# Performance work log

Hardware: AMD Instinct MI355X
Metric: run time of the kernel (lower is better)

## Reference

```python
import jax, jax.numpy as jnp
import numpy as np

N = 4096
D = 2048   # latent_dim
H = 2048   # projector hidden
P = 128    # projection dim
TEMP = 0.1
SIGMA = 5.0
GAMMA = 1.0 / (2.0 * SIGMA ** 2)
INF = 1.0e8
BN_EPS = 1e-5


def setup_inputs() -> dict:
    key = jax.random.key(0)
    k1, k2, k3, k4, k5 = jax.random.split(key, 5)
    return {
        "y1": jax.random.normal(k1, (N, D), jnp.float32),
        "y2": jax.random.normal(k2, (N, D), jnp.float32),
        "labels": jax.random.normal(k3, (N,), jnp.float32),
        "W1": jax.random.normal(k4, (H, D), jnp.float32) * 0.02,
        "bn_gamma": jnp.ones((H,), jnp.float32),
        "bn_beta": jnp.zeros((H,), jnp.float32),
        "W2": jax.random.normal(k5, (P, H), jnp.float32) * 0.02,
    }


def _project(x, W1, bn_gamma, bn_beta, W2):
    # Linear(no bias) -> BatchNorm1d (training: batch stats, biased var) -> ReLU -> Linear(no bias)
    h = x @ W1.T                                   # [N, H]
    mu = jnp.mean(h, axis=0)
    var = jnp.mean((h - mu) ** 2, axis=0)          # biased variance, as torch BN
    h = (h - mu) * jax.lax.rsqrt(var + BN_EPS) * bn_gamma + bn_beta
    h = jax.nn.relu(h)
    return h @ W2.T                                # [N, P]


def reference(y1, y2, labels, W1, bn_gamma, bn_beta, W2):
    z_i = _project(y1, W1, bn_gamma, bn_beta, W2)
    z_j = _project(y2, W1, bn_gamma, bn_beta, W2)
    n = z_i.shape[0]

    # L2 normalize
    z_i = z_i / jnp.linalg.norm(z_i, axis=-1, keepdims=True)
    z_j = z_j / jnp.linalg.norm(z_j, axis=-1, keepdims=True)

    eye_n = jnp.eye(n, dtype=z_i.dtype)
    sim_zii = z_i @ z_i.T / TEMP - INF * eye_n     # [N, N]
    sim_zjj = z_j @ z_j.T / TEMP - INF * eye_n
    sim_zij = z_i @ z_j.T / TEMP

    # RBF kernel weights over duplicated labels (sigma > 0 path)
    all_labels = jnp.concatenate([labels, labels]).reshape(2 * n, -1)   # [2N, L]
    sq_dist = jnp.sum((all_labels[:, None, :] - all_labels[None, :, :]) ** 2, axis=-1)
    weights = jnp.exp(-GAMMA * sq_dist)            # [2N, 2N]
    weights = weights * (1.0 - jnp.eye(2 * n, dtype=weights.dtype))
    weights = weights / jnp.sum(weights, axis=1, keepdims=True)

    sim_Z = jnp.concatenate([
        jnp.concatenate([sim_zii, sim_zij], axis=1),
        jnp.concatenate([sim_zij.T, sim_zjj], axis=1),
    ], axis=0)                                     # [2N, 2N]
    log_sim_Z = jax.nn.log_softmax(sim_Z, axis=1)
    loss = -jnp.sum(weights * log_sim_Z) / n
    return loss
```

## Files before the change

kernel.cpp:

```cpp
#include <hip/hip_runtime.h>

typedef unsigned short u16;
typedef unsigned int   u32;
typedef float  f32x4  __attribute__((ext_vector_type(4)));
typedef short  s16x8  __attribute__((ext_vector_type(8)));
typedef __bf16 bf16x8 __attribute__((ext_vector_type(8)));

#define GAMMA_C 0.02f
#define NSPLIT 16

__device__ __forceinline__ float bf2f(u16 h) {
  union { u32 u; float f; } c; c.u = ((u32)h) << 16; return c.f;
}
__device__ __forceinline__ u16 f2bf(float f) {
  union { float f; u32 u; } c; c.f = f;
  u32 u = c.u;
  return (u16)((u + 0x7fffu + ((u >> 16) & 1u)) >> 16);
}
__device__ __forceinline__ f32x4 mfma16(s16x8 a, s16x8 b, f32x4 c) {
  union { s16x8 s; bf16x8 b; } ua, ub; ua.s = a; ub.s = b;
  return __builtin_amdgcn_mfma_f32_16x16x32_bf16(ua.b, ub.b, c, 0, 0, 0);
}
__device__ __forceinline__ void gload_lds16(const void* g, void* l) {
  __builtin_amdgcn_global_load_lds(
      (__attribute__((address_space(1))) const void*)g,
      (__attribute__((address_space(3))) void*)l, 16, 0, 0);
}

__global__ __launch_bounds__(256)
void castall(const float* __restrict__ y1, const float* __restrict__ y2,
             const float* __restrict__ W1, const float* __restrict__ W2,
             u16* __restrict__ Ybf, u16* __restrict__ W1bf,
             u16* __restrict__ W2bf, float* __restrict__ zbuf) {
  int b = blockIdx.x;
  if (b >= 10368) {
    int i = ((b - 10368) * 256 + threadIdx.x) * 4;
    *(float4*)(zbuf + i) = make_float4(0.f, 0.f, 0.f, 0.f);
    return;
  }
  const float* src; u16* dst; int off;
  if (b < 4096)       { src = y1; dst = Ybf;           off = b; }
  else if (b < 8192)  { src = y2; dst = Ybf + 8388608; off = b - 4096; }
  else if (b < 10240) { src = W1; dst = W1bf;          off = b - 8192; }
  else                { src = W2; dst = W2bf;          off = b - 10240; }
  int idx = (off * 256 + threadIdx.x) * 8;
  float4 a = *(const float4*)(src + idx);
  float4 c = *(const float4*)(src + idx + 4);
  int4 ov; u16* op = (u16*)&ov;
  op[0]=f2bf(a.x); op[1]=f2bf(a.y); op[2]=f2bf(a.z); op[3]=f2bf(a.w);
  op[4]=f2bf(c.x); op[5]=f2bf(c.y); op[6]=f2bf(c.z); op[7]=f2bf(c.w);
  *(int4*)(dst + idx) = ov;
}

#define SWZ1(row) (((row) & 7) << 4)
#define BAR() __builtin_amdgcn_s_barrier()
#define VMW0() asm volatile("s_waitcnt vmcnt(0)" ::: "memory")

#define STAGE_T(BUF, KT) do {                                                      \
  _Pragma("unroll")                                                                \
  for (int c_ = 0; c_ < 4; ++c_) {                                                 \
    int e_ = tid + c_*512; int row_ = e_ >> 3; int b_ = (e_ & 7) * 16;             \
    int bs_ = b_ ^ SWZ1(row_);                                                     \
    gload_lds16((const char*)A + (size_t)(tm+row_)*4096 + (KT)*2 + bs_,            \
                (char*)&As[BUF][0] + (c_*512 + wave*64)*16);                       \
    gload_lds16((const char*)B + (size_t)(tn+row_)*4096 + (KT)*2 + bs_,            \
                (char*)&Bs[BUF][0] + (c_*512 + wave*64)*16);                       \
  }                                                                                \
} while (0)

#define LDA(DST, BUF, MH) do {                                                     \
  _Pragma("unroll")                                                                \
  for (int m_ = 0; m_ < 4; ++m_)                                                   \
    _Pragma("unroll")                                                              \
    for (int kk_ = 0; kk_ < 2; ++kk_) {                                            \
      int arow_ = wr*16 + ((MH)*4 + m_)*32 + r16;                                  \
      DST[m_*2 + kk_] = *(const s16x8*)((const char*)&As[BUF][0] + arow_*128 +     \
                          ((kk_*64 + g*16) ^ SWZ1(arow_)));                        \
    }                                                                              \
} while (0)

#define LDB(DST, BUF, NH) do {                                                     \
  _Pragma("unroll")                                                                \
  for (int n_ = 0; n_ < 2; ++n_)                                                   \
    _Pragma("unroll")                                                              \
    for (int kk_ = 0; kk_ < 2; ++kk_) {                                            \
      int brow_ = wc*16 + ((NH)*2 + n_)*64 + r16;                                  \
      DST[n_*2 + kk_] = *(const s16x8*)((const char*)&Bs[BUF][0] + brow_*128 +     \
                          ((kk_*64 + g*16) ^ SWZ1(brow_)));                        \
    }                                                                              \
} while (0)

#define MMQ(AF, MH, NH) do {                                                       \
  __builtin_amdgcn_s_setprio(1);                                                   \
  _Pragma("unroll")                                                                \
  for (int m_ = 0; m_ < 4; ++m_)                                                   \
    _Pragma("unroll")                                                              \
    for (int n_ = 0; n_ < 2; ++n_)                                                 \
      _Pragma("unroll")                                                            \
      for (int kk_ = 0; kk_ < 2; ++kk_)                                            \
        acc[(MH)*4 + m_][(NH)*2 + n_] =                                            \
          mfma16(AF[m_*2 + kk_], bv[n_*2 + kk_], acc[(MH)*4 + m_][(NH)*2 + n_]);   \
  __builtin_amdgcn_s_setprio(0);                                                   \
} while (0)

__global__ __launch_bounds__(512, 2)
void gemm1(const u16* __restrict__ A, const u16* __restrict__ B,
           u16* __restrict__ C, float* __restrict__ psum, float* __restrict__ psumsq)
{
  __shared__ u16 As[2][256*64];
  __shared__ u16 Bs[2][256*64];
  const int tid = threadIdx.x;
  const int lane = tid & 63, wave = tid >> 6;
  const int wr = wave >> 2, wc = wave & 3;
  const int g = lane >> 4, r16 = lane & 15;
  const int lin = blockIdx.x;
  const int wgid = (lin & 7) * 32 + (lin >> 3);
  const int by = wgid >> 3, bx = wgid & 7;
  const int tm = by * 256, tn = bx * 256;

  f32x4 acc[8][4] = {};
  s16x8 af0[8], af1[8], bv[4];

  STAGE_T(0, 0);
  VMW0(); BAR();

  for (int t = 0; t < 32; ++t) {
    const int cur = t & 1, nxt = cur ^ 1;
    const int ktn = (t + 1) * 64;
    LDA(af0, cur, 0);  LDB(bv, cur, 0);
    if (t < 31) STAGE_T(nxt, ktn);
    BAR();  MMQ(af0, 0, 0);  BAR();
    LDA(af1, cur, 1);
    BAR();  MMQ(af1, 1, 0);  BAR();
    LDB(bv, cur, 1);
    BAR();  MMQ(af1, 1, 1);  BAR();
    if (t < 31) VMW0();
    BAR();  MMQ(af0, 0, 1);  BAR();
  }

  #pragma unroll
  for (int m = 0; m < 8; ++m)
    #pragma unroll
    for (int n = 0; n < 4; ++n)
      #pragma unroll
      for (int r = 0; r < 4; ++r) {
        int row = tm + wr*16 + m*32 + g*4 + r;
        int col = tn + wc*16 + n*64 + r16;
        C[(size_t)row*2048 + col] = f2bf(acc[m][n][r]);
      }

  __syncthreads();
  float* sred  = (float*)&As[0][0];
  float* ssred = sred + 512;
  #pragma unroll
  for (int n = 0; n < 4; ++n) {
    float s = 0.f, ss = 0.f;
    #pragma unroll
    for (int m = 0; m < 8; ++m)
      #pragma unroll
      for (int r = 0; r < 4; ++r) { float v = acc[m][n][r]; s += v; ss = fmaf(v, v, ss); }
    s  += __shfl_xor(s, 16);  s  += __shfl_xor(s, 32);
    ss += __shfl_xor(ss, 16); ss += __shfl_xor(ss, 32);
    if (g == 0) {
      int lc = wc*16 + n*64 + r16;
      sred [wr*256 + lc] = s;
      ssred[wr*256 + lc] = ss;
    }
  }
  __syncthreads();
  if (tid < 256) {
    int half = tm >> 12;
    atomicAdd(&psum  [half*2048 + tn + tid], sred [tid] + sred [256 + tid]);
    atomicAdd(&psumsq[half*2048 + tn + tid], ssred[tid] + ssred[256 + tid]);
  }
}

__global__ __launch_bounds__(256)
void bnfinal(const float* __restrict__ psum, const float* __restrict__ psumsq,
             const float* __restrict__ gam, const float* __restrict__ bet,
             float* __restrict__ scale, float* __restrict__ bias)
{
  int c = blockIdx.x * 256 + threadIdx.x;
  int col = c & 2047;
  float mu  = psum[c] * (1.f/4096.f);
  float var = fmaxf(psumsq[c] * (1.f/4096.f) - mu*mu, 0.f);
  float sc = gam[col] * rsqrtf(var + 1e-5f);
  scale[c] = sc;
  bias [c] = bet[col] - mu * sc;
}

__global__ __launch_bounds__(256)
void gemm2f(const u16* __restrict__ Hraw, const u16* __restrict__ W2bf,
            const float* __restrict__ scale, const float* __restrict__ bias,
            u16* __restrict__ Zp, int kLen)
{
  __shared__ u16 As[128*64];
  __shared__ u16 Bs[128*64];
  const int tid = threadIdx.x;
  const int lane = tid & 63, wave = tid >> 6;
  const int wr = wave >> 1, wc = wave & 1;
  const int g = lane >> 4, r16 = lane & 15;
  const int tm = blockIdx.y * 128, tn = blockIdx.x * 128;
  const int kOff = blockIdx.z * kLen;
  const float* scp = scale + (size_t)(tm >> 12) * 2048;
  const float* bip = bias  + (size_t)(tm >> 12) * 2048;

  f32x4 acc[4][4] = {};

  for (int kt = kOff; kt < kOff + kLen; kt += 64) {
    #pragma unroll
    for (int c = 0; c < 4; ++c) {
      int ld = (tid + c*256) * 16;
      int row = ld >> 7, b = ld & 127;
      int bs = b ^ ((row & 7) << 4);
      gload_lds16((const char*)W2bf + (size_t)(tn+row)*4096 + (kt*2 + bs),
                  (char*)Bs + (wave*64 + c*256)*16);
    }
    #pragma unroll
    for (int c = 0; c < 4; ++c) {
      int ld = (tid + c*256) * 16;
      int row = ld >> 7, b = ld & 127;
      int kg = kt + (b >> 1);
      int4 hv = *(const int4*)((const char*)Hraw + (size_t)(tm+row)*4096 + kt*2 + b);
      f32x4 s0 = *(const f32x4*)(scp + kg), s1 = *(const f32x4*)(scp + kg + 4);
      f32x4 b0 = *(const f32x4*)(bip + kg), b1 = *(const f32x4*)(bip + kg + 4);
      u16* hp = (u16*)&hv;
      int4 ov; u16* op = (u16*)&ov;
      #pragma unroll
      for (int j = 0; j < 4; ++j)
        op[j]   = f2bf(fmaxf(fmaf(bf2f(hp[j]),   s0[j], b0[j]), 0.f));
      #pragma unroll
      for (int j = 0; j < 4; ++j)
        op[4+j] = f2bf(fmaxf(fmaf(bf2f(hp[4+j]), s1[j], b1[j]), 0.f));
      *(int4*)((char*)As + row*128 + (b ^ ((row & 7) << 4))) = ov;
    }
    __syncthreads();
    #pragma unroll
    for (int kk = 0; kk < 2; ++kk) {
      s16x8 af[4], bv[4];
      #pragma unroll
      for (int m = 0; m < 4; ++m) {
        int row = wr*64 + m*16 + r16;
        af[m] = *(const s16x8*)((const char*)As + row*128 +
                                ((kk*64 + g*16) ^ ((row & 7) << 4)));
      }
      #pragma unroll
      for (int n = 0; n < 4; ++n) {
        int row = wc*64 + n*16 + r16;
        bv[n] = *(const s16x8*)((const char*)Bs + row*128 +
                                ((kk*64 + g*16) ^ ((row & 7) << 4)));
      }
      #pragma unroll
      for (int m = 0; m < 4; ++m)
        #pragma unroll
        for (int n = 0; n < 4; ++n)
          acc[m][n] = mfma16(af[m], bv[n], acc[m][n]);
    }
    __syncthreads();
  }

  u16* Cfo = Zp + (size_t)blockIdx.z * (8192*128);
  #pragma unroll
  for (int m = 0; m < 4; ++m)
    #pragma unroll
    for (int n = 0; n < 4; ++n)
      #pragma unroll
      for (int r = 0; r < 4; ++r) {
        int row = tm + wr*64 + m*16 + g*4 + r;
        int col = tn + wc*64 + n*16 + r16;
        Cfo[(size_t)row*128 + col] = f2bf(acc[m][n][r]);
      }
}

__global__ __launch_bounds__(256)
void normk(const u16* __restrict__ Zp, u16* __restrict__ Zb)
{
  int row = blockIdx.x * 16 + (threadIdx.x >> 4);
  int l16 = threadIdx.x & 15;
  size_t off = (size_t)row*128 + l16*8;
  f32x4 v0 = {0.f,0.f,0.f,0.f}, v1 = {0.f,0.f,0.f,0.f};
  #pragma unroll
  for (int s = 0; s < 8; ++s) {
    int4 pv = *(const int4*)(Zp + (size_t)s*1048576 + off);
    const u16* pp = (const u16*)&pv;
    v0[0] += bf2f(pp[0]); v0[1] += bf2f(pp[1]); v0[2] += bf2f(pp[2]); v0[3] += bf2f(pp[3]);
    v1[0] += bf2f(pp[4]); v1[1] += bf2f(pp[5]); v1[2] += bf2f(pp[6]); v1[3] += bf2f(pp[7]);
  }
  float ss = v0[0]*v0[0] + v0[1]*v0[1] + v0[2]*v0[2] + v0[3]*v0[3]
           + v1[0]*v1[0] + v1[1]*v1[1] + v1[2]*v1[2] + v1[3]*v1[3];
  #pragma unroll
  for (int o = 1; o < 16; o <<= 1) ss += __shfl_xor(ss, o);
  float rs = rsqrtf(ss);
  rs = rs * (1.5f - 0.5f * ss * rs * rs);
  int4 ov; u16* op = (u16*)&ov;
  op[0]=f2bf(v0[0]*rs); op[1]=f2bf(v0[1]*rs); op[2]=f2bf(v0[2]*rs); op[3]=f2bf(v0[3]*rs);
  op[4]=f2bf(v1[0]*rs); op[5]=f2bf(v1[1]*rs); op[6]=f2bf(v1[2]*rs); op[7]=f2bf(v1[3]*rs);
  *(int4*)((char*)Zb + off*2) = ov;
}

#define LOAD_COL(DC, DL, IT) do {                                                  \
  int jr_ = colBase + (IT)*16;                                                     \
  const char* zcp_ = (const char*)Zb + (size_t)(jr_ + r16)*256 + g*16;             \
  DC[0] = *(const s16x8*)(zcp_);        DC[1] = *(const s16x8*)(zcp_ +  64);       \
  DC[2] = *(const s16x8*)(zcp_ + 128);  DC[3] = *(const s16x8*)(zcp_ + 192);       \
  DL = *(const f32x4*)(labels + ((jr_ & 4095) + g*4));                             \
} while (0)

#define LBODY(CC, CL, IT) do {                                                     \
  int jrow_ = colBase + (IT)*16;                                                   \
  f32x4 acc0 = {0.f,0.f,0.f,0.f};                                                  \
  f32x4 acc1 = {0.f,0.f,0.f,0.f};                                                  \
  acc0 = mfma16(CC[0], zr[0][0], acc0);                                            \
  acc0 = mfma16(CC[1], zr[0][1], acc0);                                            \
  acc0 = mfma16(CC[2], zr[0][2], acc0);                                            \
  acc0 = mfma16(CC[3], zr[0][3], acc0);                                            \
  acc1 = mfma16(CC[0], zr[1][0], acc1);                                            \
  acc1 = mfma16(CC[1], zr[1][1], acc1);                                            \
  acc1 = mfma16(CC[2], zr[1][2], acc1);                                            \
  acc1 = mfma16(CC[3], zr[1][3], acc1);                                            \
  _Pragma("unroll")                                                                \
  for (int r = 0; r < 4; ++r) {                                                    \
    int j = jrow_ + g*4 + r;                                                       \
    _Pragma("unroll")                                                              \
    for (int is = 0; is < 2; ++is) {                                               \
      float d = (is ? acc1[r] : acc0[r]);                                          \
      bool diag = (rowBase + is*16 + r16) == j;                                    \
      float e  = __expf(fmaf(d, 10.f, -10.f));                                     \
      float dl = li[is] - CL[r];                                                   \
      float w  = __expf(-GAMMA_C * dl * dl);                                       \
      e = diag ? 0.f : e;                                                          \
      w = diag ? 0.f : w;                                                          \
      l[is] += e;                                                                  \
      wS[is] += w;                                                                 \
      wA[is] = fmaf(w, d, wA[is]);                                                 \
    }                                                                              \
  }                                                                                \
} while (0)

__global__ __launch_bounds__(64)
void lossk(const u16* __restrict__ Zb, const float* __restrict__ labels,
           float* __restrict__ lacc, float* __restrict__ wacc,
           float* __restrict__ sacc)
{
  const int lane = threadIdx.x & 63;
  const int g = lane >> 4, r16 = lane & 15;
  const int split = blockIdx.x;
  const int rowBase = blockIdx.y * 32;
  const int colBase = split * 512;

  s16x8 zr[2][4];
  float li[2];
  #pragma unroll
  for (int is = 0; is < 2; ++is) {
    int i = rowBase + is*16 + r16;
    li[is] = labels[i & 4095];
    #pragma unroll
    for (int kk = 0; kk < 4; ++kk)
      zr[is][kk] = *(const s16x8*)((const char*)Zb + (size_t)i*256 + kk*64 + g*16);
  }

  float l[2]  = {0.f, 0.f};
  float wA[2] = {0.f, 0.f};
  float wS[2] = {0.f, 0.f};

  s16x8 cA[4], cB[4];
  f32x4 lA, lB;
  LOAD_COL(cA, lA, 0);
  for (int it = 0; it < 32; it += 2) {
    LOAD_COL(cB, lB, it + 1);
    LBODY(cA, lA, it);
    if (it + 2 < 32) LOAD_COL(cA, lA, it + 2);
    LBODY(cB, lB, it + 1);
  }

  #pragma unroll
  for (int is = 0; is < 2; ++is) {
    float lv = l[is], wv = wA[is], sv = wS[is];
    lv += __shfl_xor(lv, 16); lv += __shfl_xor(lv, 32);
    wv += __shfl_xor(wv, 16); wv += __shfl_xor(wv, 32);
    sv += __shfl_xor(sv, 16); sv += __shfl_xor(sv, 32);
    if (g == 0) {
      int i = rowBase + is*16 + r16;
      atomicAdd(&lacc[i], lv);
      atomicAdd(&wacc[i], wv);
      atomicAdd(&sacc[i], sv);
    }
  }
}

__global__ __launch_bounds__(256)
void finalk(const float* __restrict__ lacc, const float* __restrict__ wacc,
            const float* __restrict__ sacc, float* __restrict__ out)
{
  __shared__ float red[256];
  float a = 0.f;
  for (int i = threadIdx.x; i < 8192; i += 256)
    a += wacc[i] * 10.f / sacc[i] - (10.f + logf(lacc[i]));
  red[threadIdx.x] = a;
  __syncthreads();
  for (int off = 128; off > 0; off >>= 1) {
    if (threadIdx.x < off) red[threadIdx.x] += red[threadIdx.x + off];
    __syncthreads();
  }
  if (threadIdx.x == 0) out[0] = -red[0] * (1.f/4096.f);
}

extern "C" void kernel_launch(void* const* d_in, const int* in_sizes, int n_in,
                              void* d_out, int out_size, void* d_ws, size_t ws_size,
                              hipStream_t stream) {
  const float* y1     = (const float*)d_in[0];
  const float* y2     = (const float*)d_in[1];
  const float* labels = (const float*)d_in[2];
  const float* W1     = (const float*)d_in[3];
  const float* bng    = (const float*)d_in[4];
  const float* bnb    = (const float*)d_in[5];
  const float* W2     = (const float*)d_in[6];
  float* out = (float*)d_out;
  char* ws = (char*)d_ws;

  u16*   Ybf    = (u16*)(ws);
  u16*   W1bf   = (u16*)(ws + 33554432);
  float* zbuf   = (float*)(ws + 41943040);
  float* psum   = (float*)(ws + 41943040);
  float* psumsq = (float*)(ws + 41959424);
  float* lacc   = (float*)(ws + 41975808);
  float* wacc   = (float*)(ws + 42008576);
  float* sacc   = (float*)(ws + 42041344);
  u16*   W2bf   = (u16*)(ws + 42074112);
  u16*   Hraw   = (u16*)(ws + 42598400);
  u16*   Zp     = (u16*)(ws + 32768);
  float* scale  = (float*)(ws + 33554432);
  float* biasv  = (float*)(ws + 33570816);
  u16*   Zbf    = (u16*)(ws + 33587200);

  castall<<<10400, 256, 0, stream>>>(y1, y2, W1, W2, Ybf, W1bf, W2bf, zbuf);
  gemm1<<<256, 512, 0, stream>>>(Ybf, W1bf, Hraw, psum, psumsq);
  bnfinal<<<16, 256, 0, stream>>>(psum, psumsq, bng, bnb, scale, biasv);
  gemm2f<<<dim3(1,64,8), 256, 0, stream>>>(Hraw, W2bf, scale, biasv, Zp, 256);
  normk<<<512, 256, 0, stream>>>(Zp, Zbf);
  lossk<<<dim3(NSPLIT, 256), 64, 0, stream>>>(Zbf, labels, lacc, wacc, sacc);
  finalk<<<1, 256, 0, stream>>>(lacc, wacc, sacc, out);
}
```

Measured before the change: 187.2 us.

## Fuse BN finalize into gemm2 prologue and widen loss kernel row tile

Removes the separate bnfinal launch: each gemm2f block now computes BN scale/bias for its 256-wide K slice from psum/psumsq into shared memory and reads them from LDS instead of global. Separately, the loss kernel now processes 64 rows per block (4 row subtiles) instead of 32, so each loaded column fragment feeds twice as many MFMAs and the grid halves. The cost is redundant BN computation across blocks, more registers per lane in lossk, and half as many loss blocks to spread over the CUs.

```diff
diff --git a/kernel.cpp b/kernel.cpp
--- a/kernel.cpp
+++ b/kernel.cpp
@@ -176,34 +176,31 @@
 }
 
 __global__ __launch_bounds__(256)
-void bnfinal(const float* __restrict__ psum, const float* __restrict__ psumsq,
-             const float* __restrict__ gam, const float* __restrict__ bet,
-             float* __restrict__ scale, float* __restrict__ bias)
-{
-  int c = blockIdx.x * 256 + threadIdx.x;
-  int col = c & 2047;
-  float mu  = psum[c] * (1.f/4096.f);
-  float var = fmaxf(psumsq[c] * (1.f/4096.f) - mu*mu, 0.f);
-  float sc = gam[col] * rsqrtf(var + 1e-5f);
-  scale[c] = sc;
-  bias [c] = bet[col] - mu * sc;
-}
-
-__global__ __launch_bounds__(256)
 void gemm2f(const u16* __restrict__ Hraw, const u16* __restrict__ W2bf,
-            const float* __restrict__ scale, const float* __restrict__ bias,
+            const float* __restrict__ psum, const float* __restrict__ psumsq,
+            const float* __restrict__ gam, const float* __restrict__ bet,
             u16* __restrict__ Zp, int kLen)
 {
   __shared__ u16 As[128*64];
   __shared__ u16 Bs[128*64];
+  __shared__ float sLDS[256], bLDS[256];
   const int tid = threadIdx.x;
   const int lane = tid & 63, wave = tid >> 6;
   const int wr = wave >> 1, wc = wave & 1;
   const int g = lane >> 4, r16 = lane & 15;
   const int tm = blockIdx.y * 128, tn = blockIdx.x * 128;
   const int kOff = blockIdx.z * kLen;
-  const float* scp = scale + (size_t)(tm >> 12) * 2048;
-  const float* bip = bias  + (size_t)(tm >> 12) * 2048;
+  const int half = tm >> 12;
+
+  {
+    int c = half*2048 + kOff + tid;
+    float mu  = psum[c] * (1.f/4096.f);
+    float var = fmaxf(psumsq[c] * (1.f/4096.f) - mu*mu, 0.f);
+    float sc = gam[kOff + tid] * rsqrtf(var + 1e-5f);
+    sLDS[tid] = sc;
+    bLDS[tid] = bet[kOff + tid] - mu * sc;
+  }
+  __syncthreads();
 
   f32x4 acc[4][4] = {};
 
@@ -220,10 +217,10 @@
     for (int c = 0; c < 4; ++c) {
       int ld = (tid + c*256) * 16;
       int row = ld >> 7, b = ld & 127;
-      int kg = kt + (b >> 1);
+      int kg = (kt - kOff) + (b >> 1);
       int4 hv = *(const int4*)((const char*)Hraw + (size_t)(tm+row)*4096 + kt*2 + b);
-      f32x4 s0 = *(const f32x4*)(scp + kg), s1 = *(const f32x4*)(scp + kg + 4);
-      f32x4 b0 = *(const f32x4*)(bip + kg), b1 = *(const f32x4*)(bip + kg + 4);
+      f32x4 s0 = *(const f32x4*)(sLDS + kg), s1 = *(const f32x4*)(sLDS + kg + 4);
+      f32x4 b0 = *(const f32x4*)(bLDS + kg), b1 = *(const f32x4*)(bLDS + kg + 4);
       u16* hp = (u16*)&hv;
       int4 ov; u16* op = (u16*)&ov;
       #pragma unroll
@@ -308,22 +305,19 @@
 
 #define LBODY(CC, CL, IT) do {                                                     \
   int jrow_ = colBase + (IT)*16;                                                   \
-  f32x4 acc0 = {0.f,0.f,0.f,0.f};                                                  \
-  f32x4 acc1 = {0.f,0.f,0.f,0.f};                                                  \
-  acc0 = mfma16(CC[0], zr[0][0], acc0);                                            \
-  acc0 = mfma16(CC[1], zr[0][1], acc0);                                            \
-  acc0 = mfma16(CC[2], zr[0][2], acc0);                                            \
-  acc0 = mfma16(CC[3], zr[0][3], acc0);                                            \
-  acc1 = mfma16(CC[0], zr[1][0], acc1);                                            \
-  acc1 = mfma16(CC[1], zr[1][1], acc1);                                            \
-  acc1 = mfma16(CC[2], zr[1][2], acc1);                                            \
-  acc1 = mfma16(CC[3], zr[1][3], acc1);                                            \
+  f32x4 aacc[4] = {};                                                              \
+  _Pragma("unroll")                                                                \
+  for (int kk = 0; kk < 4; ++kk) {                                                 \
+    _Pragma("unroll")                                                              \
+    for (int is = 0; is < 4; ++is)                                                 \
+      aacc[is] = mfma16(CC[kk], zr[is][kk], aacc[is]);                             \
+  }                                                                                \
   _Pragma("unroll")                                                                \
   for (int r = 0; r < 4; ++r) {                                                    \
     int j = jrow_ + g*4 + r;                                                       \
     _Pragma("unroll")                                                              \
-    for (int is = 0; is < 2; ++is) {                                               \
-      float d = (is ? acc1[r] : acc0[r]);                                          \
+    for (int is = 0; is < 4; ++is) {                                               \
+      float d = aacc[is][r];                                                       \
       bool diag = (rowBase + is*16 + r16) == j;                                    \
       float e  = __expf(fmaf(d, 10.f, -10.f));                                     \
       float dl = li[is] - CL[r];                                                   \
@@ -345,13 +339,13 @@
   const int lane = threadIdx.x & 63;
   const int g = lane >> 4, r16 = lane & 15;
   const int split = blockIdx.x;
-  const int rowBase = blockIdx.y * 32;
+  const int rowBase = blockIdx.y * 64;
   const int colBase = split * 512;
 
-  s16x8 zr[2][4];
-  float li[2];
-  #pragma unroll
-  for (int is = 0; is < 2; ++is) {
+  s16x8 zr[4][4];
+  float li[4];
+  #pragma unroll
+  for (int is = 0; is < 4; ++is) {
     int i = rowBase + is*16 + r16;
     li[is] = labels[i & 4095];
     #pragma unroll
@@ -359,9 +353,9 @@
       zr[is][kk] = *(const s16x8*)((const char*)Zb + (size_t)i*256 + kk*64 + g*16);
   }
 
-  float l[2]  = {0.f, 0.f};
-  float wA[2] = {0.f, 0.f};
-  float wS[2] = {0.f, 0.f};
+  float l[4]  = {0.f, 0.f, 0.f, 0.f};
+  float wA[4] = {0.f, 0.f, 0.f, 0.f};
+  float wS[4] = {0.f, 0.f, 0.f, 0.f};
 
   s16x8 cA[4], cB[4];
   f32x4 lA, lB;
@@ -374,7 +368,7 @@
   }
 
   #pragma unroll
-  for (int is = 0; is < 2; ++is) {
+  for (int is = 0; is < 4; ++is) {
     float lv = l[is], wv = wA[is], sv = wS[is];
     lv += __shfl_xor(lv, 16); lv += __shfl_xor(lv, 32);
     wv += __shfl_xor(wv, 16); wv += __shfl_xor(wv, 32);
@@ -429,15 +423,12 @@
   u16*   W2bf   = (u16*)(ws + 42074112);
   u16*   Hraw   = (u16*)(ws + 42598400);
   u16*   Zp     = (u16*)(ws + 32768);
-  float* scale  = (float*)(ws + 33554432);
-  float* biasv  = (float*)(ws + 33570816);
   u16*   Zbf    = (u16*)(ws + 33587200);
 
   castall<<<10400, 256, 0, stream>>>(y1, y2, W1, W2, Ybf, W1bf, W2bf, zbuf);
   gemm1<<<256, 512, 0, stream>>>(Ybf, W1bf, Hraw, psum, psumsq);
-  bnfinal<<<16, 256, 0, stream>>>(psum, psumsq, bng, bnb, scale, biasv);
-  gemm2f<<<dim3(1,64,8), 256, 0, stream>>>(Hraw, W2bf, scale, biasv, Zp, 256);
+  gemm2f<<<dim3(1,64,8), 256, 0, stream>>>(Hraw, W2bf, psum, psumsq, bng, bnb, Zp, 256);
   normk<<<512, 256, 0, stream>>>(Zp, Zbf);
-  lossk<<<dim3(NSPLIT, 256), 64, 0, stream>>>(Zbf, labels, lacc, wacc, sacc);
+  lossk<<<dim3(NSPLIT, 128), 64, 0, stream>>>(Zbf, labels, lacc, wacc, sacc);
   finalk<<<1, 256, 0, stream>>>(lacc, wacc, sacc, out);
 }
```

Result: faster. 160.4 us (-14.3%).
